# Optimization experiments

Measured on AMD Instinct MI355X. Metric: run time of the kernel, lower is better.

Reference implementation:

```python
import jax, jax.numpy as jnp
import numpy as np

NUM_HEADS = 16
NUM_KV_HEADS = 4
ROPE_BASE = 10000.0
TRAIN_SEQ_LEN = 1024


def _rms_norm(x):
    eps = jnp.finfo(x.dtype).eps
    var = jnp.mean(jnp.square(x), axis=-1, keepdims=True)
    return x * jax.lax.rsqrt(var + eps)


def _rotary_cos_sin(seq_len, head_dim, dtype):
    # NTK-by-parts base scaling when seq_len > train_seq_len (matches Rotary.forward)
    if seq_len > TRAIN_SEQ_LEN:
        scale = seq_len / TRAIN_SEQ_LEN
        base = ROPE_BASE * scale ** (head_dim / (head_dim - 2))
    else:
        base = ROPE_BASE
    inv_freq = 1.0 / base ** (jnp.arange(0, head_dim, 2, dtype=jnp.float32) / head_dim)
    t = jnp.arange(seq_len, dtype=jnp.float32)
    freqs = jnp.outer(t, inv_freq)  # [S, head_dim//2]
    return jnp.cos(freqs).astype(dtype), jnp.sin(freqs).astype(dtype)


def _apply_rotary(x, cos, sin):
    # x: [B,S,H,D]; cos/sin: [S, D//2] broadcast over batch and heads
    half = x.shape[-1] // 2
    x1, x2 = x[..., :half], x[..., half:]
    c = cos[None, :, None, :]
    s = sin[None, :, None, :]
    return jnp.concatenate((x1 * c + x2 * s, -x1 * s + x2 * c), axis=-1)


def setup_inputs() -> dict:
    key = jax.random.key(0)
    ks = jax.random.split(key, 5)
    B, S, D = 2, 2048, 2048
    KVD = NUM_KV_HEADS * (D // NUM_HEADS)
    x = jax.random.normal(ks[0], (B, S, D), dtype=jnp.float32)
    Wq = jax.random.normal(ks[1], (D, D), dtype=jnp.float32) * 0.02
    Wk = jax.random.normal(ks[2], (KVD, D), dtype=jnp.float32) * 0.02
    Wv = jax.random.normal(ks[3], (KVD, D), dtype=jnp.float32) * 0.02
    Wproj = jax.random.normal(ks[4], (D, D), dtype=jnp.float32) * 0.02
    q_gain = jnp.ones((NUM_HEADS,), dtype=jnp.float32)
    return {"x": x, "Wq": Wq, "Wk": Wk, "Wv": Wv, "Wproj": Wproj, "q_gain": q_gain}


def reference(x, Wq, Wk, Wv, Wproj, q_gain):
    B, S, D = x.shape
    H, KH = NUM_HEADS, NUM_KV_HEADS
    hd = D // H
    group = H // KH

    q = (x @ Wq.T).reshape(B, S, H, hd)
    k = (x @ Wk.T).reshape(B, S, KH, hd)
    v = (x @ Wv.T).reshape(B, S, KH, hd)

    q = _rms_norm(q)
    k = _rms_norm(k)

    cos, sin = _rotary_cos_sin(S, hd, q.dtype)
    q = _apply_rotary(q, cos, sin)
    k = _apply_rotary(k, cos, sin)

    q = q * q_gain.astype(q.dtype)[None, None, :, None]

    # GQA: query head h attends to kv head h // group
    k = jnp.repeat(k, group, axis=2)  # [B,S,H,hd]
    v = jnp.repeat(v, group, axis=2)

    scale = 1.0 / jnp.sqrt(jnp.asarray(hd, dtype=q.dtype))
    scores = jnp.einsum("bshd,bthd->bhst", q, k) * scale  # [B,H,S,S]
    causal = jnp.tril(jnp.ones((S, S), dtype=bool))
    scores = jnp.where(causal[None, None], scores, jnp.asarray(-jnp.inf, scores.dtype))
    probs = jax.nn.softmax(scores, axis=-1)
    out = jnp.einsum("bhst,bthd->bshd", probs, v)  # [B,S,H,hd]

    return out.reshape(B, S, D) @ Wproj.T
```

## Files before the change

kernel.cpp:

```cpp
#include <hip/hip_runtime.h>
#include <cmath>

typedef unsigned short u16;
typedef short v8s __attribute__((ext_vector_type(8)));
typedef float v4f __attribute__((ext_vector_type(4)));
typedef unsigned short v4u __attribute__((ext_vector_type(4)));
typedef unsigned int v2u __attribute__((ext_vector_type(2)));

__device__ __forceinline__ u16 f2bf(float f) {
  unsigned u = __builtin_bit_cast(unsigned, f);
  u += 0x7fffu + ((u >> 16) & 1u);
  return (u16)(u >> 16);
}
__device__ __forceinline__ float bf2f(u16 h) {
  unsigned u = ((unsigned)h) << 16;
  return __builtin_bit_cast(float, u);
}
__device__ __forceinline__ unsigned pk2(float a, float b) {
  return (unsigned)f2bf(a) | ((unsigned)f2bf(b) << 16);
}

__global__ void k_cast_bf16(const float* __restrict__ in, u16* __restrict__ out, int n4) {
  int i = blockIdx.x * blockDim.x + threadIdx.x;
  if (i >= n4) return;
  v4f v = ((const v4f*)in)[i];
  v4u o;
  o[0] = f2bf(v[0]); o[1] = f2bf(v[1]); o[2] = f2bf(v[2]); o[3] = f2bf(v[3]);
  ((v4u*)out)[i] = o;
}

__global__ void k_cast_w(const float* __restrict__ a, const float* __restrict__ b,
                         const float* __restrict__ c, const float* __restrict__ d,
                         u16* __restrict__ oa, u16* __restrict__ ob, u16* __restrict__ oc,
                         u16* __restrict__ od, int na4, int nb4, int nc4, int nd4) {
  int j = blockIdx.x * blockDim.x + threadIdx.x;
  const float* src;
  u16* dst;
  if (j < na4) { src = a; dst = oa; }
  else {
    j -= na4;
    if (j < nb4) { src = b; dst = ob; }
    else {
      j -= nb4;
      if (j < nc4) { src = c; dst = oc; }
      else {
        j -= nc4;
        if (j >= nd4) return;
        src = d; dst = od;
      }
    }
  }
  v4f v = ((const v4f*)src)[j];
  v4u o;
  o[0] = f2bf(v[0]); o[1] = f2bf(v[1]); o[2] = f2bf(v[2]); o[3] = f2bf(v[3]);
  ((v4u*)dst)[j] = o;
}

__global__ void k_rope_tab(float* __restrict__ cosT, float* __restrict__ sinT, float log2_base) {
  int idx = blockIdx.x * blockDim.x + threadIdx.x;
  int t = idx >> 6, i = idx & 63;
  float inv = exp2f(-(float)i * (1.0f / 64.0f) * log2_base);
  float fr = (float)t * inv;
  cosT[idx] = cosf(fr);
  sinT[idx] = sinf(fr);
}

__global__ void k_rmsnorm_rope(u16* __restrict__ qk, const float* __restrict__ cosT,
                               const float* __restrict__ sinT, const float* __restrict__ gain,
                               int H, int S, float oscale) {
  int row = blockIdx.x * 4 + (threadIdx.x >> 6);
  int l = threadIdx.x & 63;
  int h = row % H;
  int m = row / H;
  int s = m % S;
  u16* p = qk + (size_t)row * 128;
  float a = bf2f(p[l]), b = bf2f(p[64 + l]);
  float ss = a * a + b * b;
#pragma unroll
  for (int o = 32; o; o >>= 1) ss += __shfl_xor(ss, o, 64);
  float r = rsqrtf(ss * (1.0f / 128.0f) + 1.1920929e-7f);
  a *= r; b *= r;
  float c = cosT[s * 64 + l], sn = sinT[s * 64 + l];
  float o1 = a * c + b * sn;
  float o2 = b * c - a * sn;
  float g = oscale;
  if (gain != nullptr) g *= gain[h];
  p[l] = f2bf(o1 * g);
  p[64 + l] = f2bf(o2 * g);
}

__global__ __launch_bounds__(256) void k_gemm_qkv(const u16* __restrict__ A,
                                                  const u16* __restrict__ Bw,
                                                  u16* __restrict__ q_o, u16* __restrict__ k_o,
                                                  u16* __restrict__ v_o, int M, int K) {
  __shared__ u16 sA[128 * 32];
  __shared__ u16 sB[128 * 32];
  const int tid = threadIdx.x;
  const int w = tid >> 6, l = tid & 63;
  const int lr = l & 15, lh = l >> 4;
  const int wr = w >> 1, wc = w & 1;
  const int nwg = gridDim.x * gridDim.y;
  const int bid = blockIdx.y * gridDim.x + blockIdx.x;
  const int cpx = nwg >> 3;
  const int swz = (bid & 7) * cpx + (bid >> 3);
  const int row0 = (swz / gridDim.x) * 128, col0 = (swz % gridDim.x) * 128;
  v4f zz = {0.f, 0.f, 0.f, 0.f};
  v4f acc[4][4];
#pragma unroll
  for (int mi = 0; mi < 4; ++mi)
#pragma unroll
    for (int ni = 0; ni < 4; ++ni) acc[mi][ni] = zz;

  const int lrow = l >> 2;
  const int lcol = (l & 3) * 8;

  for (int k0 = 0; k0 < K; k0 += 32) {
#pragma unroll
    for (int i = 0; i < 2; ++i) {
      int c = i * 4 + w;
      const u16* srcA = A + (size_t)(row0 + c * 16 + lrow) * K + (k0 + lcol);
      const u16* srcB = Bw + (size_t)(col0 + c * 16 + lrow) * K + (k0 + lcol);
      __builtin_amdgcn_global_load_lds((const __attribute__((address_space(1))) void*)srcA,
                                       (__attribute__((address_space(3))) void*)(sA + c * 512),
                                       16, 0, 0);
      __builtin_amdgcn_global_load_lds((const __attribute__((address_space(1))) void*)srcB,
                                       (__attribute__((address_space(3))) void*)(sB + c * 512),
                                       16, 0, 0);
    }
    __syncthreads();
    v8s af[4], bfr[4];
#pragma unroll
    for (int mi = 0; mi < 4; ++mi)
      af[mi] = *(const v8s*)(sA + (wr * 64 + mi * 16 + lr) * 32 + lh * 8);
#pragma unroll
    for (int ni = 0; ni < 4; ++ni)
      bfr[ni] = *(const v8s*)(sB + (wc * 64 + ni * 16 + lr) * 32 + lh * 8);
#pragma unroll
    for (int mi = 0; mi < 4; ++mi)
#pragma unroll
      for (int ni = 0; ni < 4; ++ni)
        acc[mi][ni] = __builtin_amdgcn_mfma_f32_16x16x32_bf16(af[mi], bfr[ni], acc[mi][ni], 0, 0, 0);
    __syncthreads();
  }
  u16* outp;
  int ldo = 0, cb;
  bool tr = false;
  if (col0 < 2048) { outp = q_o; ldo = 2048; cb = col0; }
  else if (col0 < 2560) { outp = k_o; ldo = 512; cb = col0 - 2048; }
  else { outp = v_o; tr = true; cb = col0 - 2560; }
#pragma unroll
  for (int mi = 0; mi < 4; ++mi) {
#pragma unroll
    for (int ni = 0; ni < 4; ++ni) {
      int row = row0 + wr * 64 + mi * 16 + lh * 4;
      int col = cb + wc * 64 + ni * 16 + lr;
#pragma unroll
      for (int r = 0; r < 4; ++r) {
        u16 bv = f2bf(acc[mi][ni][r]);
        if (tr) outp[(size_t)col * M + row + r] = bv;
        else    outp[(size_t)(row + r) * ldo + col] = bv;
      }
    }
  }
}

__global__ __launch_bounds__(256) void k_gemm_bt(const u16* __restrict__ A,
                                                 const u16* __restrict__ Bw,
                                                 float* __restrict__ C, int M, int N, int K) {
  __shared__ u16 sA[128 * 32];
  __shared__ u16 sB[128 * 32];
  const int tid = threadIdx.x;
  const int w = tid >> 6, l = tid & 63;
  const int lr = l & 15, lh = l >> 4;
  const int wr = w >> 1, wc = w & 1;
  const int nwg = gridDim.x * gridDim.y;
  const int bid = blockIdx.y * gridDim.x + blockIdx.x;
  const int cpx = nwg >> 3;
  const int swz = (bid & 7) * cpx + (bid >> 3);
  const int row0 = (swz / gridDim.x) * 128, col0 = (swz % gridDim.x) * 128;
  v4f zz = {0.f, 0.f, 0.f, 0.f};
  v4f acc[4][4];
#pragma unroll
  for (int mi = 0; mi < 4; ++mi)
#pragma unroll
    for (int ni = 0; ni < 4; ++ni) acc[mi][ni] = zz;

  const int lrow = l >> 2;
  const int lcol = (l & 3) * 8;

  for (int k0 = 0; k0 < K; k0 += 32) {
#pragma unroll
    for (int i = 0; i < 2; ++i) {
      int c = i * 4 + w;
      const u16* srcA = A + (size_t)(row0 + c * 16 + lrow) * K + (k0 + lcol);
      const u16* srcB = Bw + (size_t)(col0 + c * 16 + lrow) * K + (k0 + lcol);
      __builtin_amdgcn_global_load_lds((const __attribute__((address_space(1))) void*)srcA,
                                       (__attribute__((address_space(3))) void*)(sA + c * 512),
                                       16, 0, 0);
      __builtin_amdgcn_global_load_lds((const __attribute__((address_space(1))) void*)srcB,
                                       (__attribute__((address_space(3))) void*)(sB + c * 512),
                                       16, 0, 0);
    }
    __syncthreads();
    v8s af[4], bfr[4];
#pragma unroll
    for (int mi = 0; mi < 4; ++mi)
      af[mi] = *(const v8s*)(sA + (wr * 64 + mi * 16 + lr) * 32 + lh * 8);
#pragma unroll
    for (int ni = 0; ni < 4; ++ni)
      bfr[ni] = *(const v8s*)(sB + (wc * 64 + ni * 16 + lr) * 32 + lh * 8);
#pragma unroll
    for (int mi = 0; mi < 4; ++mi)
#pragma unroll
      for (int ni = 0; ni < 4; ++ni)
        acc[mi][ni] = __builtin_amdgcn_mfma_f32_16x16x32_bf16(af[mi], bfr[ni], acc[mi][ni], 0, 0, 0);
    __syncthreads();
  }
#pragma unroll
  for (int mi = 0; mi < 4; ++mi) {
#pragma unroll
    for (int ni = 0; ni < 4; ++ni) {
      int row = row0 + wr * 64 + mi * 16 + lh * 4;
      int col = col0 + wc * 64 + ni * 16 + lr;
#pragma unroll
      for (int r = 0; r < 4; ++r) C[(size_t)(row + r) * N + col] = acc[mi][ni][r];
    }
  }
}

__global__ __launch_bounds__(256) void k_flash_attn(const u16* __restrict__ Q,
                                                    const u16* __restrict__ Kb,
                                                    const u16* __restrict__ Vt,
                                                    u16* __restrict__ O, int S, int H, int KH,
                                                    int Mtot) {
  const int bh = blockIdx.x;
  const int h = bh % H, b = bh / H;
  const int kvh = h / (H / KH);
  const int w = threadIdx.x >> 6, l = threadIdx.x & 63;
  const int lr = l & 15, lh = l >> 4;

  __shared__ alignas(16) char sK[2][16384];
  __shared__ alignas(16) char sV[2][16384];
  __shared__ alignas(16) unsigned P_lds[4][16 * 32];
  unsigned* prow = P_lds[w] + lr * 32;
  const int xr = (lr & 7) << 2;

  v4f zz = {0.f, 0.f, 0.f, 0.f};
  const int strideK = KH * 128;
  const int strideKB = strideK * 2;
  const char* KheadB = (const char*)Kb + 2 * ((size_t)b * S * strideK + (size_t)kvh * 128);
  const char* VheadB = (const char*)Vt + 2 * ((size_t)(kvh * 128) * Mtot + (size_t)b * S);
  const size_t MtotB = (size_t)Mtot * 2;

  auto stage = [&](int kv0, int bufi) {
    const char* Kt = KheadB + (size_t)kv0 * strideKB;
#pragma unroll
    for (int j = 0; j < 4; ++j) {
      int jj = w * 4 + j;
      int ci = jj * 64 + l;
      int r = ci >> 4;
      int bc = (ci & 15) << 4;
      const char* src = Kt + (size_t)r * strideKB + (bc ^ ((r & 15) << 4));
      __builtin_amdgcn_global_load_lds((const __attribute__((address_space(1))) void*)src,
                                       (__attribute__((address_space(3))) void*)(sK[bufi] + jj * 1024),
                                       16, 0, 0);
    }
    const char* Vt0 = VheadB + (size_t)kv0 * 2;
#pragma unroll
    for (int j = 0; j < 4; ++j) {
      int jj = w * 4 + j;
      int ci = jj * 64 + l;
      int r = ci >> 3;
      int bc = (ci & 7) << 4;
      const char* src = Vt0 + (size_t)r * MtotB + (bc ^ ((r & 7) << 4));
      __builtin_amdgcn_global_load_lds((const __attribute__((address_space(1))) void*)src,
                                       (__attribute__((address_space(3))) void*)(sV[bufi] + jj * 1024),
                                       16, 0, 0);
    }
  };

  for (int pp = 0; pp < 2; ++pp) {
    const int qt = (pp == 0) ? (int)blockIdx.y : (S / 64 - 1 - (int)blockIdx.y);
    const int q0 = qt * 64;
    const int nt = qt + 1;
    const int qi = q0 + w * 16 + lr;

    v8s qf[4];
    const u16* qp = Q + (size_t)(b * S + q0 + w * 16 + lr) * (size_t)(H * 128) + h * 128 + lh * 8;
#pragma unroll
    for (int c = 0; c < 4; ++c) qf[c] = *(const v8s*)(qp + c * 32);

    v4f o_acc[8];
#pragma unroll
    for (int df = 0; df < 8; ++df) o_acc[df] = zz;
    float m_run = -1e30f, l_run = 0.f;

    stage(0, 0);
    __syncthreads();

    int buf = 0;
    for (int t = 0; t < nt; ++t) {
      const int kv0 = t * 64;
      const bool lastTile = (t == nt - 1);
      const char* sKb = sK[buf];
      const char* sVb = sV[buf];

      v4f sv[4];
      __builtin_amdgcn_s_setprio(1);
#pragma unroll
      for (int nf = 0; nf < 4; ++nf) {
        v4f a_ = zz;
        const int r = nf * 16 + lr;
#pragma unroll
        for (int c = 0; c < 4; ++c) {
          v8s kf = *(const v8s*)(sKb + r * 256 + ((lh * 16 + c * 64) ^ (lr << 4)));
          a_ = __builtin_amdgcn_mfma_f32_16x16x32_bf16(kf, qf[c], a_, 0, 0, 0);
        }
        sv[nf] = a_;
      }
      __builtin_amdgcn_s_setprio(0);

      if (t + 1 < nt) stage(kv0 + 64, buf ^ 1);

      if (lastTile) {
#pragma unroll
        for (int nf = 0; nf < 4; ++nf)
#pragma unroll
          for (int r = 0; r < 4; ++r)
            if (kv0 + nf * 16 + lh * 4 + r > qi) sv[nf][r] = -1e30f;
      }
      float pmax = -1e30f;
#pragma unroll
      for (int nf = 0; nf < 4; ++nf)
#pragma unroll
        for (int r = 0; r < 4; ++r) pmax = fmaxf(pmax, sv[nf][r]);
      pmax = fmaxf(pmax, __shfl_xor(pmax, 16, 64));
      pmax = fmaxf(pmax, __shfl_xor(pmax, 32, 64));
      if (!__all(pmax - m_run <= 8.0f)) {
        float mnew = fmaxf(m_run, pmax);
        float corr = exp2f(m_run - mnew);
        l_run *= corr;
        m_run = mnew;
        float corrq[4];
#pragma unroll
        for (int r = 0; r < 4; ++r) corrq[r] = __shfl(corr, lh * 4 + r, 16);
#pragma unroll
        for (int df = 0; df < 8; ++df)
#pragma unroll
          for (int r = 0; r < 4; ++r) o_acc[df][r] *= corrq[r];
      }
      float rsum = 0.f;
#pragma unroll
      for (int nf = 0; nf < 4; ++nf)
#pragma unroll
        for (int r = 0; r < 4; ++r) {
          float pv = exp2f(sv[nf][r] - m_run);
          sv[nf][r] = pv;
          rsum += pv;
        }
      rsum += __shfl_xor(rsum, 16, 64);
      rsum += __shfl_xor(rsum, 32, 64);
      l_run += rsum;

#pragma unroll
      for (int nf = 0; nf < 4; ++nf) {
        v2u pw;
        pw[0] = pk2(sv[nf][0], sv[nf][1]);
        pw[1] = pk2(sv[nf][2], sv[nf][3]);
        *(v2u*)(prow + ((nf * 8 + lh * 2) ^ xr)) = pw;
      }
      asm volatile("s_waitcnt lgkmcnt(0)" ::: "memory");
      __builtin_amdgcn_sched_barrier(0);
      v8s ap[2];
#pragma unroll
      for (int c2 = 0; c2 < 2; ++c2) ap[c2] = *(const v8s*)(prow + ((c2 * 16 + lh * 4) ^ xr));

      __builtin_amdgcn_s_setprio(1);
#pragma unroll
      for (int df = 0; df < 8; ++df) {
        const int r = df * 16 + lr;
        const char* vrow = sVb + r * 128;
        const int key = (lr & 7) << 4;
#pragma unroll
        for (int c2 = 0; c2 < 2; ++c2) {
          v8s vf = *(const v8s*)(vrow + ((lh * 16 + c2 * 64) ^ key));
          o_acc[df] = __builtin_amdgcn_mfma_f32_16x16x32_bf16(ap[c2], vf, o_acc[df], 0, 0, 0);
        }
      }
      __builtin_amdgcn_s_setprio(0);

      __syncthreads();
      buf ^= 1;
    }

    float rl = 1.0f / l_run;
    float invq[4];
#pragma unroll
    for (int r = 0; r < 4; ++r) invq[r] = __shfl(rl, lh * 4 + r, 16);
    u16* op = O + (size_t)(b * S + q0 + w * 16 + lh * 4) * (size_t)(H * 128) + h * 128;
#pragma unroll
    for (int r = 0; r < 4; ++r)
#pragma unroll
      for (int df = 0; df < 8; ++df)
        op[(size_t)r * (H * 128) + df * 16 + lr] = f2bf(o_acc[df][r] * invq[r]);
  }
}

extern "C" void kernel_launch(void* const* d_in, const int* in_sizes, int n_in, void* d_out,
                              int out_size, void* d_ws, size_t ws_size, hipStream_t stream) {
  const float* x = (const float*)d_in[0];
  const float* Wq = (const float*)d_in[1];
  const float* Wk = (const float*)d_in[2];
  const float* Wv = (const float*)d_in[3];
  const float* Wp = (const float*)d_in[4];
  const float* gain = (const float*)d_in[5];
  float* out = (float*)d_out;

  const int B = 2, S = 2048, D = 2048, H = 16, KH = 4;
  const int M = B * S;
  const int KVD = KH * 128;
  const int NQKV = D + 2 * KVD;

  char* w = (char*)d_ws;
  u16* x_bf = (u16*)w;   w += (size_t)M * D * 2;
  u16* wqkv = (u16*)w;   w += (size_t)NQKV * D * 2;
  u16* wp_bf = (u16*)w;  w += (size_t)D * D * 2;
  u16* q_bf = (u16*)w;   w += (size_t)M * D * 2;
  u16* k_bf = (u16*)w;   w += (size_t)M * KVD * 2;
  u16* v_t = (u16*)w;    w += (size_t)M * KVD * 2;
  u16* ao_bf = (u16*)w;  w += (size_t)M * D * 2;
  float* cosT = (float*)w; w += (size_t)S * 64 * 4;
  float* sinT = (float*)w; w += (size_t)S * 64 * 4;
  if ((size_t)(w - (char*)d_ws) > ws_size) return;

  k_cast_bf16<<<(M * D / 4 + 255) / 256, 256, 0, stream>>>(x, x_bf, M * D / 4);
  {
    int na4 = D * D / 4, nb4 = KVD * D / 4, nc4 = KVD * D / 4, nd4 = D * D / 4;
    int tot = na4 + nb4 + nc4 + nd4;
    k_cast_w<<<(tot + 255) / 256, 256, 0, stream>>>(
        Wq, Wk, Wv, Wp, wqkv, wqkv + (size_t)D * D, wqkv + (size_t)(D + KVD) * D, wp_bf,
        na4, nb4, nc4, nd4);
  }

  double scale = (double)S / 1024.0;
  double base = (S > 1024) ? 10000.0 * pow(scale, 128.0 / 126.0) : 10000.0;
  float l2b = (float)(log(base) / log(2.0));
  k_rope_tab<<<S * 64 / 256, 256, 0, stream>>>(cosT, sinT, l2b);

  dim3 blk(256);
  dim3 gqkv(NQKV / 128, M / 128);
  k_gemm_qkv<<<gqkv, blk, 0, stream>>>(x_bf, wqkv, q_bf, k_bf, v_t, M, D);

  float qscale = 1.4426950408889634f / sqrtf(128.0f);
  k_rmsnorm_rope<<<(M * H) / 4, 256, 0, stream>>>(q_bf, cosT, sinT, gain, H, S, qscale);
  k_rmsnorm_rope<<<(M * KH) / 4, 256, 0, stream>>>(k_bf, cosT, sinT, nullptr, KH, S, 1.0f);

  dim3 ga(B * H, S / 128);
  k_flash_attn<<<ga, blk, 0, stream>>>(q_bf, k_bf, v_t, ao_bf, S, H, KH, M);

  dim3 gp(D / 128, M / 128);
  k_gemm_bt<<<gp, blk, 0, stream>>>(ao_bf, wp_bf, out, M, D, D);
}
```

Before: 248.5 us.

## Rewrite QKV GEMM with 256x256 tiles, 8 waves, and pipelined swizzled LDS

Replaces the 128x128 QKV projection GEMM with a 512-thread kernel that computes 256x256 output tiles using K-steps of 64. LDS is double-buffered with an XOR swizzle and loads are staged in quarter-tile pieces interleaved with MFMA phases, using explicit waitcnt, barriers and setprio. The goal is more operand reuse per LDS load, fewer bank conflicts, and overlap of global loads with compute. The trade-offs are a 128KB LDS footprint, heavy register use, and a grid of only 12x16 blocks, which may leave some compute units underused.

```diff
diff --git a/kernel.cpp b/kernel.cpp
--- a/kernel.cpp
+++ b/kernel.cpp
@@ -89,59 +89,116 @@
   p[64 + l] = f2bf(o2 * g);
 }
 
-__global__ __launch_bounds__(256) void k_gemm_qkv(const u16* __restrict__ A,
-                                                  const u16* __restrict__ Bw,
-                                                  u16* __restrict__ q_o, u16* __restrict__ k_o,
-                                                  u16* __restrict__ v_o, int M, int K) {
-  __shared__ u16 sA[128 * 32];
-  __shared__ u16 sB[128 * 32];
+__device__ __forceinline__ void stage8(char* sL, const u16* __restrict__ Ag,
+                                       const u16* __restrict__ Bg, int row0, int col0, int K,
+                                       int n, int NT2, int tid) {
+  int tile = n >> 2;
+  if (tile >= NT2) return;
+  int part = n & 3;
+  int isB = (part & 1);
+  int half = (part == 1 || part == 2) ? 1 : 0;
+  const u16* src0 = isB ? Bg : Ag;
+  int g0 = (isB ? col0 : row0) + half * 128;
+  int k0 = tile * 64;
+  char* base = sL + ((tile & 1) * 65536 + isB * 32768 + half * 16384);
+#pragma unroll
+  for (int j = 0; j < 2; ++j) {
+    int o = (j * 512 + tid) * 16;
+    int rowp = o >> 8;
+    int off = o & 255;
+    int un = off ^ ((rowp & 15) << 4);
+    int rsub = rowp + ((un >> 7) << 6);
+    int k = (un & 127) >> 1;
+    const u16* src = src0 + (size_t)(g0 + rsub) * K + (k0 + k);
+    __builtin_amdgcn_global_load_lds((const __attribute__((address_space(1))) void*)src,
+                                     (__attribute__((address_space(3))) void*)(base + o), 16, 0, 0);
+  }
+}
+
+#define PH(BUF, MH, NH, LA, LB, WAITC)                                                            \
+  {                                                                                               \
+    if (LA) {                                                                                     \
+      _Pragma("unroll") for (int mi = 0; mi < 4; ++mi) {                                          \
+        _Pragma("unroll") for (int c = 0; c < 2; ++c) {                                           \
+          af[mi][c] = *(const v8s*)(sL + (BUF)*65536 + (MH)*16384 + (mi * 16 + lr) * 256 +        \
+                                    ((wm * 128 + c * 64 + lh * 16) ^ (lr << 4)));                 \
+        }                                                                                         \
+      }                                                                                           \
+    }                                                                                             \
+    if (LB) {                                                                                     \
+      _Pragma("unroll") for (int ni = 0; ni < 2; ++ni) {                                          \
+        _Pragma("unroll") for (int c = 0; c < 2; ++c) {                                           \
+          bf[ni][c] = *(const v8s*)(sL + (BUF)*65536 + 32768 + (NH)*16384 +                       \
+                                    ((wn & 1) * 32 + ni * 16 + lr) * 256 +                        \
+                                    (((wn >> 1) * 128 + c * 64 + lh * 16) ^ (lr << 4)));          \
+        }                                                                                         \
+      }                                                                                           \
+    }                                                                                             \
+    stage8(sL, Ag, Bg, row0, col0, K, n, NT2, tid);                                               \
+    ++n;                                                                                          \
+    if (WAITC) {                                                                                  \
+      if (((n - 1) >> 2) < NT2) asm volatile("s_waitcnt vmcnt(4)" ::: "memory");                  \
+      else asm volatile("s_waitcnt vmcnt(0)" ::: "memory");                                       \
+    }                                                                                             \
+    __builtin_amdgcn_sched_barrier(0);                                                            \
+    __builtin_amdgcn_s_barrier();                                                                 \
+    asm volatile("s_waitcnt lgkmcnt(0)" ::: "memory");                                            \
+    __builtin_amdgcn_sched_barrier(0);                                                            \
+    __builtin_amdgcn_s_setprio(1);                                                                \
+    _Pragma("unroll") for (int mi = 0; mi < 4; ++mi) {                                            \
+      _Pragma("unroll") for (int ni = 0; ni < 2; ++ni) {                                          \
+        _Pragma("unroll") for (int c = 0; c < 2; ++c) {                                           \
+          acc[(MH)*4 + mi][(NH)*2 + ni] = __builtin_amdgcn_mfma_f32_16x16x32_bf16(                \
+              af[mi][c], bf[ni][c], acc[(MH)*4 + mi][(NH)*2 + ni], 0, 0, 0);                      \
+        }                                                                                         \
+      }                                                                                           \
+    }                                                                                             \
+    __builtin_amdgcn_s_setprio(0);                                                                \
+    __builtin_amdgcn_sched_barrier(0);                                                            \
+    __builtin_amdgcn_s_barrier();                                                                 \
+  }
+
+__global__ __launch_bounds__(512, 2) void k_gemm_qkv8(const u16* __restrict__ Ag,
+                                                      const u16* __restrict__ Bg,
+                                                      u16* __restrict__ q_o, u16* __restrict__ k_o,
+                                                      u16* __restrict__ v_o, int M, int K) {
+  __shared__ char sL[131072];
   const int tid = threadIdx.x;
-  const int w = tid >> 6, l = tid & 63;
+  const int wid = tid >> 6, l = tid & 63;
   const int lr = l & 15, lh = l >> 4;
-  const int wr = w >> 1, wc = w & 1;
+  const int wm = wid >> 2, wn = wid & 3;
   const int nwg = gridDim.x * gridDim.y;
   const int bid = blockIdx.y * gridDim.x + blockIdx.x;
   const int cpx = nwg >> 3;
   const int swz = (bid & 7) * cpx + (bid >> 3);
-  const int row0 = (swz / gridDim.x) * 128, col0 = (swz % gridDim.x) * 128;
+  const int row0 = (swz / gridDim.x) * 256, col0 = (swz % gridDim.x) * 256;
+  const int NT2 = K >> 6;
+
   v4f zz = {0.f, 0.f, 0.f, 0.f};
-  v4f acc[4][4];
-#pragma unroll
-  for (int mi = 0; mi < 4; ++mi)
-#pragma unroll
-    for (int ni = 0; ni < 4; ++ni) acc[mi][ni] = zz;
-
-  const int lrow = l >> 2;
-  const int lcol = (l & 3) * 8;
-
-  for (int k0 = 0; k0 < K; k0 += 32) {
-#pragma unroll
-    for (int i = 0; i < 2; ++i) {
-      int c = i * 4 + w;
-      const u16* srcA = A + (size_t)(row0 + c * 16 + lrow) * K + (k0 + lcol);
-      const u16* srcB = Bw + (size_t)(col0 + c * 16 + lrow) * K + (k0 + lcol);
-      __builtin_amdgcn_global_load_lds((const __attribute__((address_space(1))) void*)srcA,
-                                       (__attribute__((address_space(3))) void*)(sA + c * 512),
-                                       16, 0, 0);
-      __builtin_amdgcn_global_load_lds((const __attribute__((address_space(1))) void*)srcB,
-                                       (__attribute__((address_space(3))) void*)(sB + c * 512),
-                                       16, 0, 0);
-    }
-    __syncthreads();
-    v8s af[4], bfr[4];
-#pragma unroll
-    for (int mi = 0; mi < 4; ++mi)
-      af[mi] = *(const v8s*)(sA + (wr * 64 + mi * 16 + lr) * 32 + lh * 8);
-#pragma unroll
-    for (int ni = 0; ni < 4; ++ni)
-      bfr[ni] = *(const v8s*)(sB + (wc * 64 + ni * 16 + lr) * 32 + lh * 8);
-#pragma unroll
-    for (int mi = 0; mi < 4; ++mi)
-#pragma unroll
-      for (int ni = 0; ni < 4; ++ni)
-        acc[mi][ni] = __builtin_amdgcn_mfma_f32_16x16x32_bf16(af[mi], bfr[ni], acc[mi][ni], 0, 0, 0);
-    __syncthreads();
-  }
+  v4f acc[8][4];
+#pragma unroll
+  for (int i = 0; i < 8; ++i)
+#pragma unroll
+    for (int j = 0; j < 4; ++j) acc[i][j] = zz;
+  v8s af[4][2], bf[2][2];
+
+  for (int i = 0; i < 6; ++i) stage8(sL, Ag, Bg, row0, col0, K, i, NT2, tid);
+  asm volatile("s_waitcnt vmcnt(4)" ::: "memory");
+  __builtin_amdgcn_sched_barrier(0);
+  __builtin_amdgcn_s_barrier();
+
+  int n = 6;
+  for (int it = 0; it < NT2 / 2; ++it) {
+    PH(0, 0, 0, 1, 1, 0)
+    PH(0, 0, 1, 0, 1, 0)
+    PH(0, 1, 1, 1, 0, 0)
+    PH(0, 1, 0, 0, 1, 1)
+    PH(1, 0, 0, 1, 1, 0)
+    PH(1, 0, 1, 0, 1, 0)
+    PH(1, 1, 1, 1, 0, 0)
+    PH(1, 1, 0, 0, 1, 1)
+  }
+
   u16* outp;
   int ldo = 0, cb;
   bool tr = false;
@@ -149,16 +206,23 @@
   else if (col0 < 2560) { outp = k_o; ldo = 512; cb = col0 - 2048; }
   else { outp = v_o; tr = true; cb = col0 - 2560; }
 #pragma unroll
-  for (int mi = 0; mi < 4; ++mi) {
-#pragma unroll
-    for (int ni = 0; ni < 4; ++ni) {
-      int row = row0 + wr * 64 + mi * 16 + lh * 4;
-      int col = cb + wc * 64 + ni * 16 + lr;
-#pragma unroll
-      for (int r = 0; r < 4; ++r) {
-        u16 bv = f2bf(acc[mi][ni][r]);
-        if (tr) outp[(size_t)col * M + row + r] = bv;
-        else    outp[(size_t)(row + r) * ldo + col] = bv;
+  for (int MH = 0; MH < 2; ++MH) {
+#pragma unroll
+    for (int mi = 0; mi < 4; ++mi) {
+#pragma unroll
+      for (int NH = 0; NH < 2; ++NH) {
+#pragma unroll
+        for (int ni = 0; ni < 2; ++ni) {
+          int row = row0 + MH * 128 + wm * 64 + mi * 16 + lh * 4;
+          int col = cb + NH * 128 + wn * 32 + ni * 16 + lr;
+          v4f a_ = acc[MH * 4 + mi][NH * 2 + ni];
+#pragma unroll
+          for (int r = 0; r < 4; ++r) {
+            u16 bv = f2bf(a_[r]);
+            if (tr) outp[(size_t)col * M + row + r] = bv;
+            else    outp[(size_t)(row + r) * ldo + col] = bv;
+          }
+        }
       }
     }
   }
@@ -447,14 +511,14 @@
   float l2b = (float)(log(base) / log(2.0));
   k_rope_tab<<<S * 64 / 256, 256, 0, stream>>>(cosT, sinT, l2b);
 
-  dim3 blk(256);
-  dim3 gqkv(NQKV / 128, M / 128);
-  k_gemm_qkv<<<gqkv, blk, 0, stream>>>(x_bf, wqkv, q_bf, k_bf, v_t, M, D);
+  dim3 gqkv(NQKV / 256, M / 256);
+  k_gemm_qkv8<<<gqkv, 512, 0, stream>>>(x_bf, wqkv, q_bf, k_bf, v_t, M, D);
 
   float qscale = 1.4426950408889634f / sqrtf(128.0f);
   k_rmsnorm_rope<<<(M * H) / 4, 256, 0, stream>>>(q_bf, cosT, sinT, gain, H, S, qscale);
   k_rmsnorm_rope<<<(M * KH) / 4, 256, 0, stream>>>(k_bf, cosT, sinT, nullptr, KH, S, 1.0f);
 
+  dim3 blk(256);
   dim3 ga(B * H, S / 128);
   k_flash_attn<<<ga, blk, 0, stream>>>(q_bf, k_bf, v_t, ao_bf, S, H, KH, M);
 
```

After: 250.3 us. Within noise of the previous version (+0.7%).
